# Optimization experiments

Hardware: AMD Instinct MI355X
Metric: run time of the kernel (lower is better)

## Reference

```python
import jax, jax.numpy as jnp
import numpy as np

B, T, K = 256, 512, 128


def setup_inputs() -> dict:
    key = jax.random.key(0)
    k1, k2, k3, k4 = jax.random.split(key, 4)
    emissions = jax.random.normal(k1, (B, T, K), jnp.float32)
    tag_ids = jax.random.randint(k2, (B, T), 0, K, dtype=jnp.int32)
    lengths = jnp.maximum(jax.random.randint(k3, (B,), 0, T + 1, dtype=jnp.int32), 1)
    # learned CRF transition matrix (transition_weight * learning_rate_multiplier)
    transitions = jax.random.normal(k4, (K, K), jnp.float32) * 0.1
    return {"emissions": emissions, "tag_ids": tag_ids, "lengths": lengths,
            "transitions": transitions}


def _log_norm(emissions, transitions, lengths):
    # forward algorithm (log-sum-exp semiring scan over time)
    t = emissions.shape[1]
    alpha0 = emissions[:, 0]  # [B,K]
    valid = jnp.arange(1, t)[:, None] < lengths[None, :]  # [T-1,B]

    def step(alpha, inp):
        emit_t, v = inp  # [B,K], [B]
        new = jax.nn.logsumexp(alpha[:, :, None] + transitions[None], axis=1) + emit_t
        return jnp.where(v[:, None], new, alpha), None

    alpha, _ = jax.lax.scan(step, alpha0, (jnp.swapaxes(emissions[:, 1:], 0, 1), valid))
    return jax.nn.logsumexp(alpha, axis=-1)  # [B]


def _sequence_score(emissions, transitions, tag_ids, lengths):
    t = emissions.shape[1]
    mask = (jnp.arange(t)[None, :] < lengths[:, None]).astype(emissions.dtype)  # [B,T]
    unary = jnp.take_along_axis(emissions, tag_ids[..., None], axis=-1)[..., 0]  # [B,T]
    unary_score = jnp.sum(unary * mask, axis=1)
    pair = transitions[tag_ids[:, :-1], tag_ids[:, 1:]]  # [B,T-1]
    binary_score = jnp.sum(pair * mask[:, 1:], axis=1)  # prefix mask: t+1 valid => t valid
    return unary_score + binary_score


def _viterbi_decode(emissions, transitions, lengths):
    t = emissions.shape[1]
    k = emissions.shape[2]
    v0 = emissions[:, 0]  # [B,K]
    valid = jnp.arange(1, t)[:, None] < lengths[None, :]  # [T-1,B]
    identity_bp = jnp.arange(k, dtype=jnp.int32)[None, :]  # pass-through for padding

    def fwd(v, inp):
        emit_t, va = inp
        scores = v[:, :, None] + transitions[None]  # [B,K,K]
        bp = jnp.argmax(scores, axis=1).astype(jnp.int32)  # [B,K]
        new = jnp.max(scores, axis=1) + emit_t
        v_new = jnp.where(va[:, None], new, v)
        bp = jnp.where(va[:, None], bp, identity_bp)
        return v_new, bp

    v_final, bps = jax.lax.scan(fwd, v0, (jnp.swapaxes(emissions[:, 1:], 0, 1), valid))
    last_tag = jnp.argmax(v_final, axis=-1).astype(jnp.int32)  # [B]

    def back(tag, bp_t):
        prev = jnp.take_along_axis(bp_t, tag[:, None], axis=1)[:, 0]
        return prev, tag  # emit tag_{t+1}, carry tag_t

    first_tag, tags_rest = jax.lax.scan(back, last_tag, bps, reverse=True)
    decoded = jnp.concatenate([first_tag[None], tags_rest], axis=0)  # [T,B]
    return jnp.swapaxes(decoded, 0, 1)  # [B,T]


def reference(emissions, tag_ids, lengths, transitions):
    log_likelihood = _sequence_score(emissions, transitions, tag_ids, lengths) \
        - _log_norm(emissions, transitions, lengths)
    loss = -jnp.mean(log_likelihood)
    decoded = _viterbi_decode(emissions, transitions, lengths)
    mask = (jnp.arange(emissions.shape[1])[None, :] < lengths[:, None]).astype(jnp.int32)
    is_equal = (tag_ids == decoded).astype(jnp.int32)
    tag_accuracy = jnp.sum(is_equal * mask) / jnp.sum(mask)
    return loss, decoded, tag_accuracy
```

## Files before the change

kernel.cpp:

```cpp
#include <hip/hip_runtime.h>

#define T_ 512
#define K_ 128
#define B_ 256

__global__ __launch_bounds__(512, 2) void crf_main(
    const float* __restrict__ emissions,
    const int* __restrict__ tag_ids,
    const int* __restrict__ lengths,
    const float* __restrict__ transitions,
    float* __restrict__ out,
    float* __restrict__ ws_ll,
    int* __restrict__ ws_cnt)
{
    __shared__ unsigned char bpLDS[T_ * K_];
    __shared__ __align__(16) float eaBuf[2][K_];
    __shared__ __align__(16) float vaBuf[2][K_];
    __shared__ __align__(16) float wmax[2][4];
    __shared__ float redLDS[8];
    __shared__ int   redILDS[8];
    __shared__ unsigned char decLDS[T_];
    __shared__ int ltagLDS;

    const int b   = blockIdx.x;
    const int tid = threadIdx.x;
    const int len = lengths[b];
    const float* emB = emissions + (size_t)b * T_ * K_;
    const int*  tagB = tag_ids + b * T_;

    {
        int t = tid;
        float s = 0.f;
        if (t < len) {
            int tg = tagB[t];
            s = emB[t * K_ + tg];
            if (t >= 1) s += transitions[tagB[t - 1] * K_ + tg];
        }
        #pragma unroll
        for (int m = 1; m < 64; m <<= 1) s += __shfl_xor(s, m);
        if ((tid & 63) == 0) redLDS[tid >> 6] = s;
    }

    const int role = tid >> 8;
    const int lin  = tid & 255;
    const int j = lin >> 1;
    const int c = lin & 1;

    float tbl[64];
    if (role == 0) {
        #pragma unroll
        for (int k = 0; k < 64; ++k)
            tbl[k] = __expf(transitions[(c * 64 + k) * K_ + j]);
    } else {
        #pragma unroll
        for (int k = 0; k < 64; ++k)
            tbl[k] = transitions[(c * 64 + k) * K_ + j];
    }

    float e0 = emB[j];
    if (role == 0) {
        if (c == 0) eaBuf[0][j] = __expf(e0);
        float wm = e0;
        #pragma unroll
        for (int m = 1; m < 64; m <<= 1) wm = fmaxf(wm, __shfl_xor(wm, m));
        if ((tid & 63) == 0) wmax[0][tid >> 6] = wm;
    } else {
        if (c == 0) vaBuf[0][j] = e0;
    }
    __syncthreads();

    int cur = 0;
    float Sprev = 0.f;
    for (int t = 1; t < len; ++t) {
        const float* em = emB + t * K_;
        if (role == 0) {
            float4 wv = *(const float4*)&wmax[cur][0];
            float Scur = fmaxf(fmaxf(wv.x, wv.y), fmaxf(wv.z, wv.w));
            float emit = em[j];
            const float* ea = &eaBuf[cur][c * 64];
            float a0 = 0.f, a1 = 0.f, a2 = 0.f, a3 = 0.f;
            #pragma unroll
            for (int k = 0; k < 16; ++k) {
                float4 e4 = *(const float4*)(ea + 4 * k);
                a0 = fmaf(e4.x, tbl[4 * k + 0], a0);
                a1 = fmaf(e4.y, tbl[4 * k + 1], a1);
                a2 = fmaf(e4.z, tbl[4 * k + 2], a2);
                a3 = fmaf(e4.w, tbl[4 * k + 3], a3);
            }
            float dot = (a0 + a1) + (a2 + a3);
            dot += __shfl_xor(dot, 1);
            float anew = __logf(dot) + Sprev + emit;
            if (c == 0) eaBuf[cur ^ 1][j] = __expf(anew - Scur);
            float wm = anew;
            #pragma unroll
            for (int m = 1; m < 64; m <<= 1) wm = fmaxf(wm, __shfl_xor(wm, m));
            if ((lin & 63) == 0) wmax[cur ^ 1][lin >> 6] = wm;
            Sprev = Scur;
        } else {
            float emit = em[j];
            const float* va = &vaBuf[cur][c * 64];
            float mB = -3.4028235e38f;
            int arg = 0;
            #pragma unroll
            for (int k = 0; k < 16; ++k) {
                float4 v4 = *(const float4*)(va + 4 * k);
                float s0 = v4.x + tbl[4 * k + 0]; if (s0 > mB) { mB = s0; arg = 4 * k + 0; }
                float s1 = v4.y + tbl[4 * k + 1]; if (s1 > mB) { mB = s1; arg = 4 * k + 1; }
                float s2 = v4.z + tbl[4 * k + 2]; if (s2 > mB) { mB = s2; arg = 4 * k + 2; }
                float s3 = v4.w + tbl[4 * k + 3]; if (s3 > mB) { mB = s3; arg = 4 * k + 3; }
            }
            arg += c * 64;
            float om = __shfl_xor(mB, 1);
            int   oa = __shfl_xor(arg, 1);
            float mLow  = c ? om : mB;   int aLow  = c ? oa : arg;
            float mHigh = c ? mB : om;   int aHigh = c ? arg : oa;
            float mF; int aF;
            if (mHigh > mLow) { mF = mHigh; aF = aHigh; } else { mF = mLow; aF = aLow; }
            if (c == 0) {
                vaBuf[cur ^ 1][j] = mF + emit;
                bpLDS[t * K_ + j] = (unsigned char)aF;
            }
        }
        cur ^= 1;
        __syncthreads();
    }

    float logZv = 0.f;
    if (tid < 64) {
        float s = eaBuf[cur][tid] + eaBuf[cur][tid + 64];
        #pragma unroll
        for (int m = 1; m < 64; m <<= 1) s += __shfl_xor(s, m);
        logZv = Sprev + __logf(s);
    }

    if (tid >= 256 && tid < 320) {
        int l = tid - 256;
        float m = vaBuf[cur][l]; int a = l;
        float v2 = vaBuf[cur][l + 64];
        if (v2 > m) { m = v2; a = l + 64; }
        #pragma unroll
        for (int sft = 1; sft < 64; sft <<= 1) {
            float om = __shfl_xor(m, sft);
            int   oa = __shfl_xor(a, sft);
            if (om > m || (om == m && oa < a)) { m = om; a = oa; }
        }
        if (l == 0) ltagLDS = a;
    }
    __syncthreads();

    if (tid == 0) {
        int tg = ltagLDS;
        for (int t = T_ - 1; t >= 1; --t) {
            decLDS[t] = (unsigned char)tg;
            if (t < len) tg = bpLDS[t * K_ + tg];
        }
        decLDS[0] = (unsigned char)tg;
    }
    __syncthreads();

    {
        int t = tid;
        int dv = decLDS[t];
        out[1 + b * T_ + t] = (float)dv;
        int good = (t < len && tagB[t] == dv) ? 1 : 0;
        #pragma unroll
        for (int m = 1; m < 64; m <<= 1) good += __shfl_xor(good, m);
        if ((tid & 63) == 0) redILDS[tid >> 6] = good;
    }
    __syncthreads();

    if (tid == 0) {
        float sc = 0.f; int cnt = 0;
        #pragma unroll
        for (int w = 0; w < 8; ++w) { sc += redLDS[w]; cnt += redILDS[w]; }
        ws_ll[b]  = sc - logZv;
        ws_cnt[b] = cnt;
    }
}

__global__ void crf_final(const float* __restrict__ ws_ll,
                          const int* __restrict__ ws_cnt,
                          const int* __restrict__ lengths,
                          float* __restrict__ out)
{
    __shared__ float sll[4];
    __shared__ int scnt[4], slen[4];
    int tid = threadIdx.x;
    float ll = ws_ll[tid];
    int   cn = ws_cnt[tid];
    int   L  = lengths[tid];
    #pragma unroll
    for (int m = 1; m < 64; m <<= 1) {
        ll += __shfl_xor(ll, m);
        cn += __shfl_xor(cn, m);
        L  += __shfl_xor(L, m);
    }
    if ((tid & 63) == 0) { sll[tid >> 6] = ll; scnt[tid >> 6] = cn; slen[tid >> 6] = L; }
    __syncthreads();
    if (tid == 0) {
        float llS = sll[0] + sll[1] + sll[2] + sll[3];
        int   cS  = scnt[0] + scnt[1] + scnt[2] + scnt[3];
        int   LS  = slen[0] + slen[1] + slen[2] + slen[3];
        out[0] = -llS / (float)B_;
        out[1 + B_ * T_] = (float)cS / (float)LS;
    }
}

extern "C" void kernel_launch(void* const* d_in, const int* in_sizes, int n_in,
                              void* d_out, int out_size, void* d_ws, size_t ws_size,
                              hipStream_t stream) {
    const float* emissions   = (const float*)d_in[0];
    const int*   tag_ids     = (const int*)d_in[1];
    const int*   lengths     = (const int*)d_in[2];
    const float* transitions = (const float*)d_in[3];
    float* out = (float*)d_out;

    float* ws_ll  = (float*)d_ws;
    int*   ws_cnt = (int*)((char*)d_ws + B_ * sizeof(float));

    crf_main<<<B_, 512, 0, stream>>>(emissions, tag_ids, lengths, transitions,
                                     out, ws_ll, ws_cnt);
    crf_final<<<1, B_, 0, stream>>>(ws_ll, ws_cnt, lengths, out);
}
```

Before: 620.3 us.

## Split each tag's reduction across four lanes with 1024-thread blocks

Doubles the block size to 1024 threads so each output tag is computed by four lanes instead of two, each handling 32 predecessors. The per-timestep serial dot product and max/argmax chain is halved, with one extra shuffle stage per step. This shortens the latency-bound recurrence at the cost of more threads per block, a heavier __syncthreads each step, and more wavefronts in the max reduction.

```diff
diff --git a/kernel.cpp b/kernel.cpp
--- a/kernel.cpp
+++ b/kernel.cpp
@@ -4,7 +4,7 @@
 #define K_ 128
 #define B_ 256
 
-__global__ __launch_bounds__(512, 2) void crf_main(
+__global__ __launch_bounds__(1024, 4) void crf_main(
     const float* __restrict__ emissions,
     const int* __restrict__ tag_ids,
     const int* __restrict__ lengths,
@@ -16,7 +16,7 @@
     __shared__ unsigned char bpLDS[T_ * K_];
     __shared__ __align__(16) float eaBuf[2][K_];
     __shared__ __align__(16) float vaBuf[2][K_];
-    __shared__ __align__(16) float wmax[2][4];
+    __shared__ __align__(16) float wmax[2][8];
     __shared__ float redLDS[8];
     __shared__ int   redILDS[8];
     __shared__ unsigned char decLDS[T_];
@@ -28,7 +28,7 @@
     const float* emB = emissions + (size_t)b * T_ * K_;
     const int*  tagB = tag_ids + b * T_;
 
-    {
+    if (tid < T_) {
         int t = tid;
         float s = 0.f;
         if (t < len) {
@@ -41,20 +41,21 @@
         if ((tid & 63) == 0) redLDS[tid >> 6] = s;
     }
 
-    const int role = tid >> 8;
-    const int lin  = tid & 255;
-    const int j = lin >> 1;
-    const int c = lin & 1;
-
-    float tbl[64];
+    const int role = tid >> 9;
+    const int lin  = tid & 511;
+    const int j = lin >> 2;
+    const int c = lin & 3;
+    const int wv = tid >> 6;
+
+    float tbl[32];
     if (role == 0) {
         #pragma unroll
-        for (int k = 0; k < 64; ++k)
-            tbl[k] = __expf(transitions[(c * 64 + k) * K_ + j]);
+        for (int k = 0; k < 32; ++k)
+            tbl[k] = __expf(transitions[(c * 32 + k) * K_ + j]);
     } else {
         #pragma unroll
-        for (int k = 0; k < 64; ++k)
-            tbl[k] = transitions[(c * 64 + k) * K_ + j];
+        for (int k = 0; k < 32; ++k)
+            tbl[k] = transitions[(c * 32 + k) * K_ + j];
     }
 
     float e0 = emB[j];
@@ -63,7 +64,7 @@
         float wm = e0;
         #pragma unroll
         for (int m = 1; m < 64; m <<= 1) wm = fmaxf(wm, __shfl_xor(wm, m));
-        if ((tid & 63) == 0) wmax[0][tid >> 6] = wm;
+        if ((lin & 63) == 0) wmax[0][wv] = wm;
     } else {
         if (c == 0) vaBuf[0][j] = e0;
     }
@@ -74,13 +75,15 @@
     for (int t = 1; t < len; ++t) {
         const float* em = emB + t * K_;
         if (role == 0) {
-            float4 wv = *(const float4*)&wmax[cur][0];
-            float Scur = fmaxf(fmaxf(wv.x, wv.y), fmaxf(wv.z, wv.w));
+            float4 w0 = *(const float4*)&wmax[cur][0];
+            float4 w1 = *(const float4*)&wmax[cur][4];
+            float Scur = fmaxf(fmaxf(fmaxf(w0.x, w0.y), fmaxf(w0.z, w0.w)),
+                               fmaxf(fmaxf(w1.x, w1.y), fmaxf(w1.z, w1.w)));
             float emit = em[j];
-            const float* ea = &eaBuf[cur][c * 64];
+            const float* ea = &eaBuf[cur][c * 32];
             float a0 = 0.f, a1 = 0.f, a2 = 0.f, a3 = 0.f;
             #pragma unroll
-            for (int k = 0; k < 16; ++k) {
+            for (int k = 0; k < 8; ++k) {
                 float4 e4 = *(const float4*)(ea + 4 * k);
                 a0 = fmaf(e4.x, tbl[4 * k + 0], a0);
                 a1 = fmaf(e4.y, tbl[4 * k + 1], a1);
@@ -89,36 +92,37 @@
             }
             float dot = (a0 + a1) + (a2 + a3);
             dot += __shfl_xor(dot, 1);
+            dot += __shfl_xor(dot, 2);
             float anew = __logf(dot) + Sprev + emit;
             if (c == 0) eaBuf[cur ^ 1][j] = __expf(anew - Scur);
             float wm = anew;
             #pragma unroll
             for (int m = 1; m < 64; m <<= 1) wm = fmaxf(wm, __shfl_xor(wm, m));
-            if ((lin & 63) == 0) wmax[cur ^ 1][lin >> 6] = wm;
+            if ((lin & 63) == 0) wmax[cur ^ 1][wv] = wm;
             Sprev = Scur;
         } else {
             float emit = em[j];
-            const float* va = &vaBuf[cur][c * 64];
+            const float* va = &vaBuf[cur][c * 32];
             float mB = -3.4028235e38f;
             int arg = 0;
             #pragma unroll
-            for (int k = 0; k < 16; ++k) {
+            for (int k = 0; k < 8; ++k) {
                 float4 v4 = *(const float4*)(va + 4 * k);
                 float s0 = v4.x + tbl[4 * k + 0]; if (s0 > mB) { mB = s0; arg = 4 * k + 0; }
                 float s1 = v4.y + tbl[4 * k + 1]; if (s1 > mB) { mB = s1; arg = 4 * k + 1; }
                 float s2 = v4.z + tbl[4 * k + 2]; if (s2 > mB) { mB = s2; arg = 4 * k + 2; }
                 float s3 = v4.w + tbl[4 * k + 3]; if (s3 > mB) { mB = s3; arg = 4 * k + 3; }
             }
-            arg += c * 64;
-            float om = __shfl_xor(mB, 1);
-            int   oa = __shfl_xor(arg, 1);
-            float mLow  = c ? om : mB;   int aLow  = c ? oa : arg;
-            float mHigh = c ? mB : om;   int aHigh = c ? arg : oa;
-            float mF; int aF;
-            if (mHigh > mLow) { mF = mHigh; aF = aHigh; } else { mF = mLow; aF = aLow; }
+            arg += c * 32;
+            #pragma unroll
+            for (int d = 1; d < 4; d <<= 1) {
+                float om = __shfl_xor(mB, d);
+                int   oa = __shfl_xor(arg, d);
+                if (om > mB || (om == mB && oa < arg)) { mB = om; arg = oa; }
+            }
             if (c == 0) {
-                vaBuf[cur ^ 1][j] = mF + emit;
-                bpLDS[t * K_ + j] = (unsigned char)aF;
+                vaBuf[cur ^ 1][j] = mB + emit;
+                bpLDS[t * K_ + j] = (unsigned char)arg;
             }
         }
         cur ^= 1;
@@ -133,8 +137,8 @@
         logZv = Sprev + __logf(s);
     }
 
-    if (tid >= 256 && tid < 320) {
-        int l = tid - 256;
+    if (tid >= 512 && tid < 576) {
+        int l = tid - 512;
         float m = vaBuf[cur][l]; int a = l;
         float v2 = vaBuf[cur][l + 64];
         if (v2 > m) { m = v2; a = l + 64; }
@@ -158,7 +162,7 @@
     }
     __syncthreads();
 
-    {
+    if (tid < T_) {
         int t = tid;
         int dv = decLDS[t];
         out[1 + b * T_ + t] = (float)dv;
@@ -218,7 +222,7 @@
     float* ws_ll  = (float*)d_ws;
     int*   ws_cnt = (int*)((char*)d_ws + B_ * sizeof(float));
 
-    crf_main<<<B_, 512, 0, stream>>>(emissions, tag_ids, lengths, transitions,
-                                     out, ws_ll, ws_cnt);
+    crf_main<<<B_, 1024, 0, stream>>>(emissions, tag_ids, lengths, transitions,
+                                      out, ws_ll, ws_cnt);
     crf_final<<<1, B_, 0, stream>>>(ws_ll, ws_cnt, lengths, out);
 }
```

After: 662.3 us. 1.07x slower.

## Split forward and Viterbi recursions into separate blocks with staged emission prefetch

Applied to the files above, without the earlier changes.

Each batch row now gets two 256-thread blocks, one running the log-sum-exp forward recursion and one running the Viterbi recursion, so the two no longer share a block-wide barrier per step. The forward pass drops the per-step wave max reduction and uses the previous step's element-0 value as the stabilizer. Emissions are staged through a double-buffered LDS tile prefetched eight steps at a time, and the barrier becomes a lighter custom s_barrier. Transition weights are held in explicitly fenced registers and the Viterbi argmax uses four independent chains. The trade-off is twice as many blocks and a less robust normalizer that could overflow or underflow if alpha values spread widely.

```diff
diff --git a/kernel.cpp b/kernel.cpp
--- a/kernel.cpp
+++ b/kernel.cpp
@@ -3,8 +3,34 @@
 #define T_ 512
 #define K_ 128
 #define B_ 256
-
-__global__ __launch_bounds__(512, 2) void crf_main(
+#define NEGINF (-3.4028235e38f)
+
+#define BAR() do { asm volatile("s_waitcnt lgkmcnt(0)" ::: "memory"); \
+                   __builtin_amdgcn_s_barrier(); \
+                   asm volatile("" ::: "memory"); } while (0)
+
+#define GR16(F) F(0) F(1) F(2) F(3) F(4) F(5) F(6) F(7) \
+                F(8) F(9) F(10) F(11) F(12) F(13) F(14) F(15)
+
+#define DECLW(g) float w##g##_0, w##g##_1, w##g##_2, w##g##_3;
+#define LOADW(g) w##g##_0 = wp[(4*g+0)*K_]; w##g##_1 = wp[(4*g+1)*K_]; \
+                 w##g##_2 = wp[(4*g+2)*K_]; w##g##_3 = wp[(4*g+3)*K_];
+#define EXPW(g)  w##g##_0 = __expf(w##g##_0); w##g##_1 = __expf(w##g##_1); \
+                 w##g##_2 = __expf(w##g##_2); w##g##_3 = __expf(w##g##_3);
+#define FENCEW(g) asm volatile("" : "+v"(w##g##_0), "+v"(w##g##_1), \
+                                    "+v"(w##g##_2), "+v"(w##g##_3));
+
+#define FG(g, acc) { float4 e_ = *(const float4*)(va + 4*g); \
+    acc = fmaf(e_.x, w##g##_0, acc); acc = fmaf(e_.y, w##g##_1, acc); \
+    acc = fmaf(e_.z, w##g##_2, acc); acc = fmaf(e_.w, w##g##_3, acc); }
+
+#define VG(g, mm, aa) { float4 e_ = *(const float4*)(va + 4*g); \
+    float s0_ = e_.x + w##g##_0; if (s0_ > mm) { mm = s0_; aa = 4*g+0; } \
+    float s1_ = e_.y + w##g##_1; if (s1_ > mm) { mm = s1_; aa = 4*g+1; } \
+    float s2_ = e_.z + w##g##_2; if (s2_ > mm) { mm = s2_; aa = 4*g+2; } \
+    float s3_ = e_.w + w##g##_3; if (s3_ > mm) { mm = s3_; aa = 4*g+3; } }
+
+__global__ __launch_bounds__(256, 2) void crf_main(
     const float* __restrict__ emissions,
     const int* __restrict__ tag_ids,
     const int* __restrict__ lengths,
@@ -13,168 +39,163 @@
     float* __restrict__ ws_ll,
     int* __restrict__ ws_cnt)
 {
-    __shared__ unsigned char bpLDS[T_ * K_];
-    __shared__ __align__(16) float eaBuf[2][K_];
-    __shared__ __align__(16) float vaBuf[2][K_];
-    __shared__ __align__(16) float wmax[2][4];
-    __shared__ float redLDS[8];
-    __shared__ int   redILDS[8];
-    __shared__ unsigned char decLDS[T_];
-    __shared__ int ltagLDS;
-
-    const int b   = blockIdx.x;
-    const int tid = threadIdx.x;
-    const int len = lengths[b];
+    __shared__ __align__(16) unsigned char smem[75328];
+    unsigned char* bp  = smem;
+    float* emLDS = (float*)(smem + 65536);
+    float* buf   = (float*)(smem + 73728);
+    unsigned char* dec = smem + 74752;
+    float* sNormF = (float*)(smem + 75264);
+    float* redS   = sNormF + 2;
+    int*   redI   = (int*)(redS + 4);
+    int*   ltag   = redI + 4;
+
+    const int bx   = blockIdx.x;
+    const int b    = bx >> 1;
+    const int role = bx & 1;
+    const int tid  = threadIdx.x;
+    const int len  = lengths[b];
     const float* emB = emissions + (size_t)b * T_ * K_;
     const int*  tagB = tag_ids + b * T_;
 
+    const int j = tid >> 1;
+    const int c = tid & 1;
+
+    GR16(DECLW)
     {
-        int t = tid;
+        const float* wp = transitions + (c * 64) * K_ + j;
+        GR16(LOADW)
+        if (role == 0) { GR16(EXPW) }
+        GR16(FENCEW)
+    }
+
+    {
+        float4 v0 = *(const float4*)&emB[tid * 4];
+        *(float4*)&emLDS[tid * 4] = v0;
+    }
+    if (role == 0) {
         float s = 0.f;
-        if (t < len) {
-            int tg = tagB[t];
-            s = emB[t * K_ + tg];
-            if (t >= 1) s += transitions[tagB[t - 1] * K_ + tg];
+        #pragma unroll
+        for (int q = 0; q < 2; ++q) {
+            int t = tid + q * 256;
+            if (t < len) {
+                int tg = tagB[t];
+                float v = emB[t * K_ + tg];
+                if (t >= 1) v += transitions[tagB[t - 1] * K_ + tg];
+                s += v;
+            }
         }
         #pragma unroll
         for (int m = 1; m < 64; m <<= 1) s += __shfl_xor(s, m);
-        if ((tid & 63) == 0) redLDS[tid >> 6] = s;
-    }
-
-    const int role = tid >> 8;
-    const int lin  = tid & 255;
-    const int j = lin >> 1;
-    const int c = lin & 1;
-
-    float tbl[64];
-    if (role == 0) {
-        #pragma unroll
-        for (int k = 0; k < 64; ++k)
-            tbl[k] = __expf(transitions[(c * 64 + k) * K_ + j]);
+        if ((tid & 63) == 0) redS[tid >> 6] = s;
+        if (tid < K_) buf[tid] = __expf(emB[tid]);
+        if (tid == 0) sNormF[0] = emB[0];
     } else {
-        #pragma unroll
-        for (int k = 0; k < 64; ++k)
-            tbl[k] = transitions[(c * 64 + k) * K_ + j];
-    }
-
-    float e0 = emB[j];
-    if (role == 0) {
-        if (c == 0) eaBuf[0][j] = __expf(e0);
-        float wm = e0;
-        #pragma unroll
-        for (int m = 1; m < 64; m <<= 1) wm = fmaxf(wm, __shfl_xor(wm, m));
-        if ((tid & 63) == 0) wmax[0][tid >> 6] = wm;
-    } else {
-        if (c == 0) vaBuf[0][j] = e0;
+        if (tid < K_) buf[tid] = emB[tid];
     }
     __syncthreads();
 
     int cur = 0;
     float Sprev = 0.f;
+    float4 stv = make_float4(0.f, 0.f, 0.f, 0.f);
     for (int t = 1; t < len; ++t) {
-        const float* em = emB + t * K_;
+        const int ph = t & 7;
+        if (ph == 1) {
+            int nc = (t >> 3) + 1;
+            if (nc < T_ / 8) {
+                stv = *(const float4*)&emB[nc * 1024 + tid * 4];
+                asm volatile("" : "+v"(stv.x), "+v"(stv.y), "+v"(stv.z), "+v"(stv.w));
+            }
+        }
+        const float* va = &buf[cur * K_ + c * 64];
+        float emit = emLDS[((t >> 3) & 1) * 1024 + ph * 128 + j];
         if (role == 0) {
-            float4 wv = *(const float4*)&wmax[cur][0];
-            float Scur = fmaxf(fmaxf(wv.x, wv.y), fmaxf(wv.z, wv.w));
-            float emit = em[j];
-            const float* ea = &eaBuf[cur][c * 64];
+            float Scur = sNormF[cur];
             float a0 = 0.f, a1 = 0.f, a2 = 0.f, a3 = 0.f;
-            #pragma unroll
-            for (int k = 0; k < 16; ++k) {
-                float4 e4 = *(const float4*)(ea + 4 * k);
-                a0 = fmaf(e4.x, tbl[4 * k + 0], a0);
-                a1 = fmaf(e4.y, tbl[4 * k + 1], a1);
-                a2 = fmaf(e4.z, tbl[4 * k + 2], a2);
-                a3 = fmaf(e4.w, tbl[4 * k + 3], a3);
-            }
+            FG(0,a0) FG(1,a1) FG(2,a2) FG(3,a3) FG(4,a0) FG(5,a1) FG(6,a2) FG(7,a3)
+            FG(8,a0) FG(9,a1) FG(10,a2) FG(11,a3) FG(12,a0) FG(13,a1) FG(14,a2) FG(15,a3)
             float dot = (a0 + a1) + (a2 + a3);
             dot += __shfl_xor(dot, 1);
-            float anew = __logf(dot) + Sprev + emit;
-            if (c == 0) eaBuf[cur ^ 1][j] = __expf(anew - Scur);
-            float wm = anew;
-            #pragma unroll
-            for (int m = 1; m < 64; m <<= 1) wm = fmaxf(wm, __shfl_xor(wm, m));
-            if ((lin & 63) == 0) wmax[cur ^ 1][lin >> 6] = wm;
+            if (c == 0) {
+                float anew = __logf(dot) + Sprev + emit;
+                buf[(cur ^ 1) * K_ + j] = __expf(anew - Scur);
+                if (j == 0) sNormF[cur ^ 1] = anew;
+            }
             Sprev = Scur;
         } else {
-            float emit = em[j];
-            const float* va = &vaBuf[cur][c * 64];
-            float mB = -3.4028235e38f;
-            int arg = 0;
+            float m0 = NEGINF, m1 = NEGINF, m2 = NEGINF, m3 = NEGINF;
+            int   a0 = 0, a1 = 0, a2 = 0, a3 = 0;
+            VG(0,m0,a0) VG(1,m0,a0) VG(2,m0,a0) VG(3,m0,a0)
+            VG(4,m1,a1) VG(5,m1,a1) VG(6,m1,a1) VG(7,m1,a1)
+            VG(8,m2,a2) VG(9,m2,a2) VG(10,m2,a2) VG(11,m2,a2)
+            VG(12,m3,a3) VG(13,m3,a3) VG(14,m3,a3) VG(15,m3,a3)
+            if (m1 > m0) { m0 = m1; a0 = a1; }
+            if (m3 > m2) { m2 = m3; a2 = a3; }
+            if (m2 > m0) { m0 = m2; a0 = a2; }
+            int arg = a0 + c * 64;
+            float om = __shfl_xor(m0, 1);
+            int   oa = __shfl_xor(arg, 1);
+            if (om > m0 || (om == m0 && oa < arg)) { m0 = om; arg = oa; }
+            if (c == 0) {
+                buf[(cur ^ 1) * K_ + j] = m0 + emit;
+                bp[t * K_ + j] = (unsigned char)arg;
+            }
+        }
+        if (ph == 6) {
+            int nc = (t >> 3) + 1;
+            if (nc < T_ / 8) *(float4*)&emLDS[(nc & 1) * 1024 + tid * 4] = stv;
+        }
+        cur ^= 1;
+        BAR();
+    }
+
+    if (role == 0) {
+        float logZv = 0.f;
+        if (tid < 64) {
+            float s = buf[cur * K_ + tid] + buf[cur * K_ + tid + 64];
             #pragma unroll
-            for (int k = 0; k < 16; ++k) {
-                float4 v4 = *(const float4*)(va + 4 * k);
-                float s0 = v4.x + tbl[4 * k + 0]; if (s0 > mB) { mB = s0; arg = 4 * k + 0; }
-                float s1 = v4.y + tbl[4 * k + 1]; if (s1 > mB) { mB = s1; arg = 4 * k + 1; }
-                float s2 = v4.z + tbl[4 * k + 2]; if (s2 > mB) { mB = s2; arg = 4 * k + 2; }
-                float s3 = v4.w + tbl[4 * k + 3]; if (s3 > mB) { mB = s3; arg = 4 * k + 3; }
-            }
-            arg += c * 64;
-            float om = __shfl_xor(mB, 1);
-            int   oa = __shfl_xor(arg, 1);
-            float mLow  = c ? om : mB;   int aLow  = c ? oa : arg;
-            float mHigh = c ? mB : om;   int aHigh = c ? arg : oa;
-            float mF; int aF;
-            if (mHigh > mLow) { mF = mHigh; aF = aHigh; } else { mF = mLow; aF = aLow; }
-            if (c == 0) {
-                vaBuf[cur ^ 1][j] = mF + emit;
-                bpLDS[t * K_ + j] = (unsigned char)aF;
-            }
-        }
-        cur ^= 1;
-        __syncthreads();
-    }
-
-    float logZv = 0.f;
-    if (tid < 64) {
-        float s = eaBuf[cur][tid] + eaBuf[cur][tid + 64];
-        #pragma unroll
-        for (int m = 1; m < 64; m <<= 1) s += __shfl_xor(s, m);
-        logZv = Sprev + __logf(s);
-    }
-
-    if (tid >= 256 && tid < 320) {
-        int l = tid - 256;
-        float m = vaBuf[cur][l]; int a = l;
-        float v2 = vaBuf[cur][l + 64];
-        if (v2 > m) { m = v2; a = l + 64; }
-        #pragma unroll
-        for (int sft = 1; sft < 64; sft <<= 1) {
-            float om = __shfl_xor(m, sft);
-            int   oa = __shfl_xor(a, sft);
-            if (om > m || (om == m && oa < a)) { m = om; a = oa; }
-        }
-        if (l == 0) ltagLDS = a;
-    }
-    __syncthreads();
-
-    if (tid == 0) {
-        int tg = ltagLDS;
-        for (int t = T_ - 1; t >= 1; --t) {
-            decLDS[t] = (unsigned char)tg;
-            if (t < len) tg = bpLDS[t * K_ + tg];
-        }
-        decLDS[0] = (unsigned char)tg;
-    }
-    __syncthreads();
-
-    {
-        int t = tid;
-        int dv = decLDS[t];
-        out[1 + b * T_ + t] = (float)dv;
-        int good = (t < len && tagB[t] == dv) ? 1 : 0;
+            for (int m = 1; m < 64; m <<= 1) s += __shfl_xor(s, m);
+            logZv = Sprev + __logf(s);
+        }
+        if (tid == 0) {
+            float sc = redS[0] + redS[1] + redS[2] + redS[3];
+            ws_ll[b] = sc - logZv;
+        }
+    } else {
+        if (tid < 64) {
+            float m = buf[cur * K_ + tid]; int a = tid;
+            float v2 = buf[cur * K_ + tid + 64];
+            if (v2 > m) { m = v2; a = tid + 64; }
+            #pragma unroll
+            for (int s = 1; s < 64; s <<= 1) {
+                float om = __shfl_xor(m, s);
+                int   oa = __shfl_xor(a, s);
+                if (om > m || (om == m && oa < a)) { m = om; a = oa; }
+            }
+            if (tid == 0) *ltag = a;
+        }
+        BAR();
+        if (tid == 0) {
+            int tg = *ltag;
+            for (int t = T_ - 1; t >= 1; --t) {
+                dec[t] = (unsigned char)tg;
+                if (t < len) tg = bp[t * K_ + tg];
+            }
+            dec[0] = (unsigned char)tg;
+        }
+        BAR();
+        int good = 0;
+        #pragma unroll
+        for (int q = 0; q < 2; ++q) {
+            int t = tid + q * 256;
+            int dv = dec[t];
+            out[1 + b * T_ + t] = (float)dv;
+            good += (t < len && tagB[t] == dv) ? 1 : 0;
+        }
         #pragma unroll
         for (int m = 1; m < 64; m <<= 1) good += __shfl_xor(good, m);
-        if ((tid & 63) == 0) redILDS[tid >> 6] = good;
-    }
-    __syncthreads();
-
-    if (tid == 0) {
-        float sc = 0.f; int cnt = 0;
-        #pragma unroll
-        for (int w = 0; w < 8; ++w) { sc += redLDS[w]; cnt += redILDS[w]; }
-        ws_ll[b]  = sc - logZv;
-        ws_cnt[b] = cnt;
+        if ((tid & 63) == 0) redI[tid >> 6] = good;
+        BAR();
+        if (tid == 0) ws_cnt[b] = redI[0] + redI[1] + redI[2] + redI[3];
     }
 }
 
@@ -218,7 +239,7 @@
     float* ws_ll  = (float*)d_ws;
     int*   ws_cnt = (int*)((char*)d_ws + B_ * sizeof(float));
 
-    crf_main<<<B_, 512, 0, stream>>>(emissions, tag_ids, lengths, transitions,
-                                     out, ws_ll, ws_cnt);
+    crf_main<<<2 * B_, 256, 0, stream>>>(emissions, tag_ids, lengths, transitions,
+                                         out, ws_ll, ws_cnt);
     crf_final<<<1, B_, 0, stream>>>(ws_ll, ws_cnt, lengths, out);
 }
```

After: 794.7 us. 1.28x slower.
